# Optimization experiments

Measured on AMD Instinct MI355X. Metric: run time of the kernel, lower is better.

## Reference

```python
import jax, jax.numpy as jnp
import numpy as np
import math

# Static config derived from init_kwargs
B, L, D, H, NL = 256, 256, 128, 2, 2
E = D // H                       # 64
F = L // 2 + 1                   # 129 rfft bins
SR = 0.6                         # sample_ratio (> 1/n_layers)
STEP = (F * (1.0 - SR)) // (NL - 1)          # 51.0, python float floor-div as in torch code
LEFTS = [int(F * (1.0 - SR) - k * STEP) for k in range(NL)]   # [51, 0]
RIGHTS = [int(F - k * STEP) for k in range(NL)]               # [129, 78]
TOPK = max(int(1 * math.log(L)), 1)          # factor=1 -> 5
NUM_TOTAL = 100000                           # user_num + item_num
SPATIAL_RATIO = 0.1
INV_SQRT_E = 1.0 / math.sqrt(E)
INV_SQRT_2 = 1.0 / math.sqrt(2.0)


def setup_inputs() -> dict:
    key = jax.random.key(0)
    ks = jax.random.split(key, 12)
    s = 0.05
    return {
        "paths": jax.random.randint(ks[0], (B, L), 0, NUM_TOTAL),
        "lengths": jax.random.randint(ks[1], (B,), 1, L + 1),
        "degrees": jax.random.randint(ks[2], (B,), 0, 64),
        "training": 1,
        "ego_emb": jax.random.normal(ks[3], (NUM_TOTAL + 1, D), jnp.float32) * s,
        "pos_emb": jax.random.normal(ks[4], (L, D), jnp.float32) * s,
        "Wq": jax.random.normal(ks[5], (NL, D, D), jnp.float32) * s,
        "Wk": jax.random.normal(ks[6], (NL, D, D), jnp.float32) * s,
        "Wv": jax.random.normal(ks[7], (NL, D, D), jnp.float32) * s,
        "Wp": jax.random.normal(ks[8], (NL, D, D), jnp.float32) * s,
        "F1": jax.random.normal(ks[9], (NL, D, 2 * D), jnp.float32) * s,
        "F2": jax.random.normal(ks[10], (NL, 2 * D, D), jnp.float32) * s,
    }


def _hybrid_attention(k, x, mask, Wq, Wk, Wv, Wp):
    # project and split heads: [B,H,E,L]
    def proj(W):
        return (x @ W).reshape(B, L, H, E).transpose(0, 2, 3, 1)
    q, kk, v = proj(Wq), proj(Wk), proj(Wv)
    qf = jnp.fft.rfft(q, axis=-1)   # [B,H,E,F] complex
    kf = jnp.fft.rfft(kk, axis=-1)
    vf = jnp.fft.rfft(v, axis=-1)
    l, r = LEFTS[k], RIGHTS[k]
    # frequency-band attention: band-limited cross-correlation (scatter back == zero-pad)
    res = qf[..., l:r] * jnp.conj(kf[..., l:r])
    box = jnp.zeros(qf.shape, dtype=res.dtype).at[..., l:r].set(res)
    corr = jnp.fft.irfft(box, n=L, axis=-1)          # [B,H,E,L]
    mean_value = jnp.mean(corr, axis=(1, 2))         # [B,L]
    # training branch: global topk delays (shared across batch), roll-based aggregation
    _, delays = jax.lax.top_k(jnp.mean(mean_value, axis=0), TOPK)   # [TOPK]
    weights = mean_value[:, delays]                  # [B,TOPK]
    tmp_corr = jax.nn.softmax(weights, axis=-1)      # [B,TOPK]
    # roll(v, -d) along time == gather at (t + d) % L
    idx = (jnp.arange(L)[None, :] + delays[:, None]) % L            # [TOPK,L]
    gathered = v[:, :, :, idx]                       # [B,H,E,TOPK,L]
    freq = jnp.einsum('bhetl,bt->bhel', gathered, tmp_corr)
    freq = freq.transpose(0, 3, 1, 2).reshape(B, L, D)
    # dual-domain: time attention on band-limited signals (std=True -> same band)
    def band_ifft(f):
        padded = jnp.zeros(f.shape, dtype=f.dtype).at[..., l:r].set(f[..., l:r])
        return jnp.fft.irfft(padded, n=L, axis=-1).transpose(0, 1, 3, 2)   # [B,H,L,E]
    qt, kt, vt = band_ifft(qf), band_ifft(kf), band_ifft(vf)
    scores = jnp.einsum('bhqe,bhke->bhqk', qt, kt) * INV_SQRT_E + mask
    att = jax.nn.softmax(scores, axis=-1)
    spatial = jnp.einsum('bhqk,bhke->bhqe', att, vt).transpose(0, 2, 1, 3).reshape(B, L, D)
    out = (1.0 - SPATIAL_RATIO) * freq + SPATIAL_RATIO * spatial
    return out @ Wp + x


def reference(paths, lengths, degrees, training, ego_emb, pos_emb, Wq, Wk, Wv, Wp, F1, F2):
    del degrees, training  # degrees unused; training branch baked in (training=True)
    x = ego_emb[paths] + pos_emb[None, :, :]         # [B,L,D]
    m = (paths < NUM_TOTAL).astype(jnp.float32)
    mask = ((1.0 - m) * -10000.0)[:, None, None, :]  # [B,1,1,L]
    for k in range(NL):
        a = _hybrid_attention(k, x, mask, Wq[k], Wk[k], Wv[k], Wp[k])
        h = a @ F1[k]
        h = h * 0.5 * (1.0 + jax.lax.erf(h * INV_SQRT_2))   # exact GELU
        x = h @ F2[k]
    # gather last valid position per sequence
    return x[jnp.arange(B), lengths - 1]             # [B,D]
```

## Files before the change

kernel.cpp:

```cpp
#include <hip/hip_runtime.h>
#include <math.h>

#define Bn 256
#define Ln 256
#define Dn 128
#define Hn 2
#define En 64
#define NLn 2
#define TOPKn 5
#define NUM_TOTALn 100000
#define BLD (Bn*Ln*Dn)
#define WT_LAYER 147456

using frag_ab = __attribute__((ext_vector_type(8))) short;
using frag_cd = __attribute__((ext_vector_type(4))) float;

__device__ inline short f2bf(float f) {
    union { float f; unsigned u; } c; c.f = f;
    unsigned r = (c.u + 0x7FFFu + ((c.u >> 16) & 1u)) >> 16;
    return (short)r;
}
__device__ inline float bf2f(short s) {
    union { unsigned u; float f; } c; c.u = ((unsigned)(unsigned short)s) << 16;
    return c.f;
}

__global__ void beacon_kernel(float* out, float v) { out[0] = v; }

__global__ __launch_bounds__(256) void build_G_kernel(short* __restrict__ G) {
    int k = blockIdx.x, t = blockIdx.y, s = threadIdx.x;
    int d = (t - s) & 255;
    int f1 = (k == 0) ? 51 : 1;
    int f2 = (k == 0) ? 127 : 77;
    float acc;
    if (d == 0) {
        acc = 2.0f * (float)(f2 - f1 + 1);
    } else {
        const float c = 3.14159265358979323846f / 256.0f;
        int ahi = (d * (2 * f2 + 1)) & 511;
        int alo = (d * (2 * f1 - 1)) & 511;
        acc = (sinf(c * (float)ahi) - sinf(c * (float)alo)) / sinf(c * (float)d);
    }
    acc += (k == 0) ? ((d & 1) ? -1.0f : 1.0f)
                    : 1.0f;
    G[((size_t)k * 256 + t) * 256 + s] = f2bf(acc * (1.0f / 256.0f));
}

__global__ __launch_bounds__(256) void build_x_kernel(const int* __restrict__ paths,
                                                      const float* __restrict__ ego,
                                                      const float* __restrict__ pos,
                                                      short* __restrict__ x) {
    int base = (blockIdx.x * 256 + threadIdx.x) * 4;
    int d = base & 127;
    int bl = base >> 7;
    int t = bl & 255;
    float4 e = *(const float4*)(ego + (size_t)paths[bl] * Dn + d);
    float4 p = *(const float4*)(pos + t * Dn + d);
    short4 s;
    s.x = f2bf(e.x + p.x); s.y = f2bf(e.y + p.y);
    s.z = f2bf(e.z + p.z); s.w = f2bf(e.w + p.w);
    *(short4*)&x[base] = s;
}

__global__ __launch_bounds__(256) void wtrans_all_kernel(
        const float* __restrict__ Wq, const float* __restrict__ Wk,
        const float* __restrict__ Wv, const float* __restrict__ Wp,
        const float* __restrict__ F1, const float* __restrict__ F2,
        short* __restrict__ Wt) {
    int z = blockIdx.y;
    int idx = blockIdx.x * 256 + threadIdx.x;
    short* WtL = Wt + (size_t)z * WT_LAYER;
    if (idx < 65536) {
        int which = idx >> 14, local = idx & 16383;
        const float* src = (which == 0) ? Wq : (which == 1) ? Wk
                         : (which == 2) ? Wv : Wp;
        float scale = (which == 3) ? 0.1f : 1.0f;
        int n = local & 127, k = local >> 7;
        WtL[(which << 14) + n * 128 + k] = f2bf(scale * src[(size_t)z * 16384 + local]);
    } else if (idx < 98304) {
        int local = idx - 65536;
        int n = local & 255, k = local >> 8;
        WtL[65536 + n * 128 + k] = f2bf(F1[(size_t)z * 32768 + local]);
    } else {
        int local = idx - 98304;
        int n = local & 127, k = local >> 7;
        WtL[98304 + n * 256 + k] = f2bf(F2[(size_t)z * 32768 + local]);
    }
}

template<bool BT_FAST, bool GELU_EPI>
__global__ __launch_bounds__(256)
void mfma_gemm_kernel(const short* A, const short* Bp, short* C, const short* R,
                      int K, int lda, int ldb, int ldc, int ldr,
                      long long sA, long long sB, long long sC, long long sR,
                      long long sCsplit, float alpha, float beta) {
    int bz = blockIdx.z;
    A += (size_t)bz * sA; C += (size_t)bz * sC;
    if (R) R += (size_t)bz * sR;
    const short* Bt = Bp + (size_t)bz * sB;
    const int m0 = blockIdx.x * 128, n0 = blockIdx.y * 128;
    int n0c = n0;
    if (sCsplit) { C += (size_t)blockIdx.y * sCsplit; n0c = 0; }
    __shared__ short As[128 * 40];
    __shared__ short Bs[128 * 40];
    int tid = threadIdx.x;
    int lane = tid & 63, wave = tid >> 6;
    int wr = (wave >> 1) * 64, wc = (wave & 1) * 64;
    int l15 = lane & 15, qd = lane >> 4;

    frag_cd zero4 = {0.f, 0.f, 0.f, 0.f};
    frag_cd acc[4][4];
    #pragma unroll
    for (int i = 0; i < 4; i++)
        #pragma unroll
        for (int j = 0; j < 4; j++) acc[i][j] = zero4;

    int arow = tid >> 1, acg = (tid & 1) * 16;
    int bnrow = tid >> 1, bcg = (tid & 1) * 16;
    int bkk = tid & 31, bnb = (tid >> 5) * 16;

    int4 pa0, pa1, pb0, pb1;
    {
        const short* ap = A + (size_t)(m0 + arow) * lda + acg;
        pa0 = *(const int4*)ap; pa1 = *(const int4*)(ap + 8);
        if (BT_FAST) {
            const short* bp = Bt + (size_t)(n0 + bnrow) * ldb + bcg;
            pb0 = *(const int4*)bp; pb1 = *(const int4*)(bp + 8);
        } else {
            const short* bp = Bt + (size_t)bkk * ldb + n0 + bnb;
            pb0 = *(const int4*)bp; pb1 = *(const int4*)(bp + 8);
        }
    }

    for (int k0 = 0; k0 < K; k0 += 32) {
        __syncthreads();
        *(int4*)&As[arow * 40 + acg] = pa0;
        *(int4*)&As[arow * 40 + acg + 8] = pa1;
        if (BT_FAST) {
            *(int4*)&Bs[bnrow * 40 + bcg] = pb0;
            *(int4*)&Bs[bnrow * 40 + bcg + 8] = pb1;
        } else {
            short tmp[16];
            *(int4*)&tmp[0] = pb0; *(int4*)&tmp[8] = pb1;
            #pragma unroll
            for (int i = 0; i < 16; i++) Bs[(bnb + i) * 40 + bkk] = tmp[i];
        }
        __syncthreads();
        if (k0 + 32 < K) {
            const short* ap = A + (size_t)(m0 + arow) * lda + k0 + 32 + acg;
            pa0 = *(const int4*)ap; pa1 = *(const int4*)(ap + 8);
            if (BT_FAST) {
                const short* bp = Bt + (size_t)(n0 + bnrow) * ldb + k0 + 32 + bcg;
                pb0 = *(const int4*)bp; pb1 = *(const int4*)(bp + 8);
            } else {
                const short* bp = Bt + (size_t)(k0 + 32 + bkk) * ldb + n0 + bnb;
                pb0 = *(const int4*)bp; pb1 = *(const int4*)(bp + 8);
            }
        }
        frag_ab af[4], bf[4];
        #pragma unroll
        for (int ms = 0; ms < 4; ms++)
            af[ms] = *(frag_ab*)&As[(wr + ms * 16 + l15) * 40 + qd * 8];
        #pragma unroll
        for (int ns = 0; ns < 4; ns++)
            bf[ns] = *(frag_ab*)&Bs[(wc + ns * 16 + l15) * 40 + qd * 8];
        #pragma unroll
        for (int ms = 0; ms < 4; ms++)
            #pragma unroll
            for (int ns = 0; ns < 4; ns++)
                acc[ms][ns] = __builtin_amdgcn_mfma_f32_16x16x32_bf16(
                    bf[ns], af[ms], acc[ms][ns], 0, 0, 0);
    }
    #pragma unroll
    for (int ms = 0; ms < 4; ms++) {
        int m = m0 + wr + ms * 16 + l15;
        #pragma unroll
        for (int ns = 0; ns < 4; ns++) {
            int nb = wc + ns * 16 + qd * 4;
            float v[4];
            #pragma unroll
            for (int r = 0; r < 4; r++) v[r] = alpha * acc[ms][ns][r];
            if (R) {
                short4 r4 = *(const short4*)&R[(size_t)m * ldr + n0 + nb];
                v[0] += beta * bf2f(r4.x); v[1] += beta * bf2f(r4.y);
                v[2] += beta * bf2f(r4.z); v[3] += beta * bf2f(r4.w);
            }
            if (GELU_EPI) {
                #pragma unroll
                for (int r = 0; r < 4; r++)
                    v[r] = v[r] * 0.5f * (1.0f + erff(v[r] * 0.70710678118654752f));
            }
            short4 o;
            o.x = f2bf(v[0]); o.y = f2bf(v[1]); o.z = f2bf(v[2]); o.w = f2bf(v[3]);
            *(short4*)&C[(size_t)m * ldc + n0c + nb] = o;
        }
    }
}

static inline void mgemm(hipStream_t s, const short* A, const short* B, short* C,
                         const short* R, int M, int N, int K,
                         int lda, int ldb, int ldc, int ldr,
                         long long sA, long long sB, long long sC, long long sR,
                         int batch, float alpha, float beta, bool btFast, bool gelu,
                         long long sCsplit = 0) {
    dim3 grid(M / 128, N / 128, batch), block(256);
    if (btFast) {
        if (gelu) mfma_gemm_kernel<true, true ><<<grid, block, 0, s>>>(A, B, C, R, K, lda, ldb, ldc, ldr, sA, sB, sC, sR, sCsplit, alpha, beta);
        else      mfma_gemm_kernel<true, false><<<grid, block, 0, s>>>(A, B, C, R, K, lda, ldb, ldc, ldr, sA, sB, sC, sR, sCsplit, alpha, beta);
    } else {
        if (gelu) mfma_gemm_kernel<false, true ><<<grid, block, 0, s>>>(A, B, C, R, K, lda, ldb, ldc, ldr, sA, sB, sC, sR, sCsplit, alpha, beta);
        else      mfma_gemm_kernel<false, false><<<grid, block, 0, s>>>(A, B, C, R, K, lda, ldb, ldc, ldr, sA, sB, sC, sR, sCsplit, alpha, beta);
    }
}

__global__ __launch_bounds__(512)
void filtproj_kernel(const short* __restrict__ G, const short* __restrict__ x,
                     const short* __restrict__ W, short* __restrict__ q) {
    int b = blockIdx.x;
    __shared__ short As[256 * 40];
    __shared__ short Bs[128 * 40];
    __shared__ short xf[256 * 136];
    int tid = threadIdx.x;
    int lane = tid & 63, wave = tid >> 6;
    int wr = (wave & 3) * 64, wc = (wave >> 2) * 64;
    int l15 = lane & 15, qd = lane >> 4;
    const short* xb = x + ((size_t)b << 15);

    frag_cd zero4 = {0.f, 0.f, 0.f, 0.f};
    frag_cd acc[4][4];
    #pragma unroll
    for (int i = 0; i < 4; i++)
        #pragma unroll
        for (int j = 0; j < 4; j++) acc[i][j] = zero4;

    int arow = tid >> 1, acg = (tid & 1) * 16;
    int bkk = tid & 31, bnb = (tid >> 5) * 16;

    int4 pa0, pa1, pb0, pb1;
    {
        const short* ap = G + (size_t)arow * 256 + acg;
        pa0 = *(const int4*)ap; pa1 = *(const int4*)(ap + 8);
        if (tid < 256) {
            const short* bp = xb + (size_t)bkk * 128 + bnb;
            pb0 = *(const int4*)bp; pb1 = *(const int4*)(bp + 8);
        }
    }
    for (int k0 = 0; k0 < 256; k0 += 32) {
        __syncthreads();
        *(int4*)&As[arow * 40 + acg] = pa0;
        *(int4*)&As[arow * 40 + acg + 8] = pa1;
        if (tid < 256) {
            short tmp[16];
            *(int4*)&tmp[0] = pb0; *(int4*)&tmp[8] = pb1;
            #pragma unroll
            for (int i = 0; i < 16; i++) Bs[(bnb + i) * 40 + bkk] = tmp[i];
        }
        __syncthreads();
        if (k0 + 32 < 256) {
            const short* ap = G + (size_t)arow * 256 + k0 + 32 + acg;
            pa0 = *(const int4*)ap; pa1 = *(const int4*)(ap + 8);
            if (tid < 256) {
                const short* bp = xb + (size_t)(k0 + 32 + bkk) * 128 + bnb;
                pb0 = *(const int4*)bp; pb1 = *(const int4*)(bp + 8);
            }
        }
        frag_ab af[4], bf[4];
        #pragma unroll
        for (int ms = 0; ms < 4; ms++)
            af[ms] = *(frag_ab*)&As[(wr + ms * 16 + l15) * 40 + qd * 8];
        #pragma unroll
        for (int ns = 0; ns < 4; ns++)
            bf[ns] = *(frag_ab*)&Bs[(wc + ns * 16 + l15) * 40 + qd * 8];
        #pragma unroll
        for (int ms = 0; ms < 4; ms++)
            #pragma unroll
            for (int ns = 0; ns < 4; ns++)
                acc[ms][ns] = __builtin_amdgcn_mfma_f32_16x16x32_bf16(
                    bf[ns], af[ms], acc[ms][ns], 0, 0, 0);
    }
    #pragma unroll
    for (int ms = 0; ms < 4; ms++) {
        int m = wr + ms * 16 + l15;
        #pragma unroll
        for (int ns = 0; ns < 4; ns++) {
            int nb = wc + ns * 16 + qd * 4;
            short4 o;
            o.x = f2bf(acc[ms][ns][0]); o.y = f2bf(acc[ms][ns][1]);
            o.z = f2bf(acc[ms][ns][2]); o.w = f2bf(acc[ms][ns][3]);
            *(short4*)&xf[m * 136 + nb] = o;
        }
    }

    int brow = tid >> 2, bcg = (tid & 3) * 8;
    #pragma unroll 1
    for (int y = 0; y < 3; y++) {
        const short* Bt = W + y * 16384;
        #pragma unroll
        for (int i = 0; i < 4; i++)
            #pragma unroll
            for (int j = 0; j < 4; j++) acc[i][j] = zero4;
        int4 pb = *(const int4*)(Bt + (size_t)brow * 128 + bcg);
        for (int k0 = 0; k0 < 128; k0 += 32) {
            __syncthreads();
            *(int4*)&Bs[brow * 40 + bcg] = pb;
            __syncthreads();
            if (k0 + 32 < 128)
                pb = *(const int4*)(Bt + (size_t)brow * 128 + k0 + 32 + bcg);
            frag_ab af[4], bf[4];
            #pragma unroll
            for (int ms = 0; ms < 4; ms++)
                af[ms] = *(frag_ab*)&xf[(wr + ms * 16 + l15) * 136 + k0 + qd * 8];
            #pragma unroll
            for (int ns = 0; ns < 4; ns++)
                bf[ns] = *(frag_ab*)&Bs[(wc + ns * 16 + l15) * 40 + qd * 8];
            #pragma unroll
            for (int ms = 0; ms < 4; ms++)
                #pragma unroll
                for (int ns = 0; ns < 4; ns++)
                    acc[ms][ns] = __builtin_amdgcn_mfma_f32_16x16x32_bf16(
                        bf[ns], af[ms], acc[ms][ns], 0, 0, 0);
        }
        short* Cy = q + (size_t)y * BLD + ((size_t)b << 15);
        #pragma unroll
        for (int ms = 0; ms < 4; ms++) {
            int m = wr + ms * 16 + l15;
            #pragma unroll
            for (int ns = 0; ns < 4; ns++) {
                int nb = wc + ns * 16 + qd * 4;
                short4 o;
                o.x = f2bf(acc[ms][ns][0]); o.y = f2bf(acc[ms][ns][1]);
                o.z = f2bf(acc[ms][ns][2]); o.w = f2bf(acc[ms][ns][3]);
                *(short4*)&Cy[(size_t)m * 128 + nb] = o;
            }
        }
    }
}

__global__ __launch_bounds__(512)
void amix_ffn_kernel(const short* __restrict__ x, const short* __restrict__ q,
                     const short* __restrict__ W,
                     const float* __restrict__ tc, const int* __restrict__ delays,
                     short* __restrict__ xout) {
    int b = blockIdx.x;
    __shared__ short aL[256 * 132];
    __shared__ short hA[256 * 132];
    __shared__ short Bs[2][128 * 40];
    int tid = threadIdx.x;
    int lane = tid & 63, wave = tid >> 6;
    int wr = (wave & 3) * 64, wc = (wave >> 2) * 64;
    int l15 = lane & 15, qd = lane >> 4;
    const short* xb = x + ((size_t)b << 15);

    float wj[TOPKn]; int dj[TOPKn];
    #pragma unroll
    for (int j = 0; j < TOPKn; j++) {
        wj[j] = tc[b * TOPKn + j];
        dj[j] = delays[j];
    }

    frag_cd zero4 = {0.f, 0.f, 0.f, 0.f};

    {
        int arow = tid >> 1, acg = (tid & 1) * 16;
        #pragma unroll
        for (int k0 = 0; k0 < 128; k0 += 32) {
            #pragma unroll
            for (int c = 0; c < 2; c++) {
                int col = k0 + acg + c * 8;
                float m8[8] = {0.f, 0.f, 0.f, 0.f, 0.f, 0.f, 0.f, 0.f};
                #pragma unroll
                for (int j = 0; j < TOPKn; j++) {
                    frag_ab v = *(const frag_ab*)(xb + (((arow + dj[j]) & 255) << 7) + col);
                    #pragma unroll
                    for (int i = 0; i < 8; i++) m8[i] += wj[j] * bf2f(v[i]);
                }
                frag_ab o;
                #pragma unroll
                for (int i = 0; i < 8; i++) o[i] = f2bf(m8[i]);
                *(frag_ab*)&hA[arow * 132 + col] = o;
            }
        }
        const short* qb = q + ((size_t)b << 15);
        #pragma unroll
        for (int p = 0; p < 8; p++) {
            int chunk = p * 512 + tid;
            int r = chunk >> 4, cb = (chunk & 15) * 8;
            *(frag_ab*)&aL[r * 132 + cb] = *(const frag_ab*)(qb + (size_t)r * 128 + cb);
        }
    }
    __syncthreads();

    int brow = tid >> 2, bcg = (tid & 3) * 8;

    frag_cd acc[4][4];
    #pragma unroll
    for (int i = 0; i < 4; i++)
        #pragma unroll
        for (int j = 0; j < 4; j++) acc[i][j] = zero4;
    #pragma unroll 1
    for (int pass = 0; pass < 2; pass++) {
        const short* Bt = W + (pass ? 49152 : 131072);
        const short* Asrc = pass ? aL : hA;
        int4 pb = *(const int4*)(Bt + (size_t)brow * 128 + bcg);
        int cur = 0;
        for (int k0 = 0; k0 < 128; k0 += 32, cur ^= 1) {
            *(int4*)&Bs[cur][brow * 40 + bcg] = pb;
            if (k0 + 32 < 128)
                pb = *(const int4*)(Bt + (size_t)brow * 128 + k0 + 32 + bcg);
            __syncthreads();
            frag_ab af[4], bf[4];
            #pragma unroll
            for (int ms = 0; ms < 4; ms++)
                af[ms] = *(frag_ab*)&Asrc[(wr + ms * 16 + l15) * 132 + k0 + qd * 8];
            #pragma unroll
            for (int ns = 0; ns < 4; ns++)
                bf[ns] = *(frag_ab*)&Bs[cur][(wc + ns * 16 + l15) * 40 + qd * 8];
            #pragma unroll
            for (int ms = 0; ms < 4; ms++)
                #pragma unroll
                for (int ns = 0; ns < 4; ns++)
                    acc[ms][ns] = __builtin_amdgcn_mfma_f32_16x16x32_bf16(
                        bf[ns], af[ms], acc[ms][ns], 0, 0, 0);
        }
    }
    __syncthreads();
    #pragma unroll
    for (int ms = 0; ms < 4; ms++) {
        int m = wr + ms * 16 + l15;
        #pragma unroll
        for (int ns = 0; ns < 4; ns++) {
            int nb = wc + ns * 16 + qd * 4;
            short4 r4 = *(const short4*)&xb[(size_t)m * 128 + nb];
            float v[4];
            v[0] = acc[ms][ns][0] + bf2f(r4.x);
            v[1] = acc[ms][ns][1] + bf2f(r4.y);
            v[2] = acc[ms][ns][2] + bf2f(r4.z);
            v[3] = acc[ms][ns][3] + bf2f(r4.w);
            short4 o;
            o.x = f2bf(v[0]); o.y = f2bf(v[1]); o.z = f2bf(v[2]); o.w = f2bf(v[3]);
            *(short4*)&aL[m * 132 + nb] = o;
        }
    }
    __syncthreads();

    const short* F1T = W + 65536;
    const short* F2T = W + 98304;
    frag_cd xacc[4][4];
    #pragma unroll
    for (int i = 0; i < 4; i++)
        #pragma unroll
        for (int j = 0; j < 4; j++) xacc[i][j] = zero4;

    #pragma unroll 1
    for (int half = 0; half < 2; half++) {
        const short* B1 = F1T + (size_t)(half * 128) * 128;
        frag_cd hacc[4][4];
        #pragma unroll
        for (int i = 0; i < 4; i++)
            #pragma unroll
            for (int j = 0; j < 4; j++) hacc[i][j] = zero4;
        {
            int4 pb = *(const int4*)(B1 + (size_t)brow * 128 + bcg);
            int cur = 0;
            for (int k0 = 0; k0 < 128; k0 += 32, cur ^= 1) {
                *(int4*)&Bs[cur][brow * 40 + bcg] = pb;
                if (k0 + 32 < 128)
                    pb = *(const int4*)(B1 + (size_t)brow * 128 + k0 + 32 + bcg);
                __syncthreads();
                frag_ab af[4], bf[4];
                #pragma unroll
                for (int ms = 0; ms < 4; ms++)
                    af[ms] = *(frag_ab*)&aL[(wr + ms * 16 + l15) * 132 + k0 + qd * 8];
                #pragma unroll
                for (int ns = 0; ns < 4; ns++)
                    bf[ns] = *(frag_ab*)&Bs[cur][(wc + ns * 16 + l15) * 40 + qd * 8];
                #pragma unroll
                for (int ms = 0; ms < 4; ms++)
                    #pragma unroll
                    for (int ns = 0; ns < 4; ns++)
                        hacc[ms][ns] = __builtin_amdgcn_mfma_f32_16x16x32_bf16(
                            bf[ns], af[ms], hacc[ms][ns], 0, 0, 0);
            }
        }
        __syncthreads();
        #pragma unroll
        for (int ms = 0; ms < 4; ms++) {
            int m = wr + ms * 16 + l15;
            #pragma unroll
            for (int ns = 0; ns < 4; ns++) {
                int nb = wc + ns * 16 + qd * 4;
                float v[4];
                #pragma unroll
                for (int r = 0; r < 4; r++) {
                    float t = hacc[ms][ns][r];
                    v[r] = t * 0.5f * (1.0f + erff(t * 0.70710678118654752f));
                }
                short4 o;
                o.x = f2bf(v[0]); o.y = f2bf(v[1]);
                o.z = f2bf(v[2]); o.w = f2bf(v[3]);
                *(short4*)&hA[m * 132 + nb] = o;
            }
        }
        __syncthreads();

        {
            int4 pb = *(const int4*)(F2T + (size_t)brow * 256 + half * 128 + bcg);
            int cur = 0;
            for (int k0 = 0; k0 < 128; k0 += 32, cur ^= 1) {
                *(int4*)&Bs[cur][brow * 40 + bcg] = pb;
                if (k0 + 32 < 128)
                    pb = *(const int4*)(F2T + (size_t)brow * 256 + half * 128 + k0 + 32 + bcg);
                __syncthreads();
                frag_ab af[4], bf[4];
                #pragma unroll
                for (int ms = 0; ms < 4; ms++)
                    af[ms] = *(frag_ab*)&hA[(wr + ms * 16 + l15) * 132 + k0 + qd * 8];
                #pragma unroll
                for (int ns = 0; ns < 4; ns++)
                    bf[ns] = *(frag_ab*)&Bs[cur][(wc + ns * 16 + l15) * 40 + qd * 8];
                #pragma unroll
                for (int ms = 0; ms < 4; ms++)
                    #pragma unroll
                    for (int ns = 0; ns < 4; ns++)
                        xacc[ms][ns] = __builtin_amdgcn_mfma_f32_16x16x32_bf16(
                            bf[ns], af[ms], xacc[ms][ns], 0, 0, 0);
            }
        }
    }
    short* xo = xout + ((size_t)b << 15);
    #pragma unroll
    for (int ms = 0; ms < 4; ms++) {
        int m = wr + ms * 16 + l15;
        #pragma unroll
        for (int ns = 0; ns < 4; ns++) {
            int nb = wc + ns * 16 + qd * 4;
            short4 o;
            o.x = f2bf(xacc[ms][ns][0]); o.y = f2bf(xacc[ms][ns][1]);
            o.z = f2bf(xacc[ms][ns][2]); o.w = f2bf(xacc[ms][ns][3]);
            *(short4*)&xo[(size_t)m * 128 + nb] = o;
        }
    }
}

__global__ __launch_bounds__(512, 4) void attn_kernel(short* q,
        const short* __restrict__ kb, const short* __restrict__ vf,
        const int* __restrict__ paths, float* __restrict__ mv2) {
    int h = blockIdx.x, b = blockIdx.y;
    __shared__ short SB[256 * 72];
    __shared__ short ks[64 * 72];
    __shared__ short vT[80 * 72];
    __shared__ float masks[256];
    __shared__ float mvpart[512];
    int tid = threadIdx.x;
    int lane = tid & 63, wave = tid >> 6;
    int l15 = lane & 15, qd = lane >> 4;
    if (tid < 256) masks[tid] = (paths[b * 256 + tid] < NUM_TOTALn) ? 0.0f : -10000.0f;
    {
        int e0 = tid * 2;
        #pragma unroll
        for (int i = 0; i < 2; i++) {
            int e = e0 + i;
            int row = 64 + (e >> 6), col = e & 63;
            vT[row * 72 + col] = (row == 64) ? (short)0x3F80 : (short)0;
        }
    }
    short* qg = q + ((size_t)b << 15) + (size_t)h * 64;
    const short* kg = kb + ((size_t)b << 15) + (size_t)h * 64;
    const short* vg = vf + ((size_t)b << 15) + (size_t)h * 64;

    #pragma unroll
    for (int p = 0; p < 4; p++) {
        int chunk = p * 512 + tid;
        int r = chunk >> 3, cb = (chunk & 7) * 8;
        *(frag_ab*)&SB[r * 72 + cb] = *(const frag_ab*)(qg + (size_t)r * 128 + cb);
    }
    __syncthreads();
    int myrow = wave * 32;
    frag_ab aq[2][2];
    #pragma unroll
    for (int mt = 0; mt < 2; mt++)
        #pragma unroll
        for (int hf = 0; hf < 2; hf++)
            aq[mt][hf] = *(frag_ab*)&SB[(myrow + mt * 16 + l15) * 72 + hf * 32 + qd * 8];

    frag_cd zero4 = {0.f, 0.f, 0.f, 0.f};
    frag_cd oacc[2][5];
    #pragma unroll
    for (int mt = 0; mt < 2; mt++)
        #pragma unroll
        for (int et = 0; et < 5; et++) oacc[mt][et] = zero4;
    float macc = 0.0f;
    int tau = tid & 255, half = tid >> 8;

    for (int jt = 0; jt < 4; jt++) {
        __syncthreads();
        {
            int r = tid >> 3, cb = (tid & 7) * 8;
            *(frag_ab*)&ks[r * 72 + cb] =
                *(const frag_ab*)(kg + (size_t)(jt * 64 + r) * 128 + cb);
            frag_ab v8 = *(const frag_ab*)(vg + (size_t)(jt * 64 + r) * 128 + cb);
            int swz = (((r >> 3) ^ (cb >> 3)) << 3) + (r & 7);
            #pragma unroll
            for (int i = 0; i < 8; i++) vT[(cb + i) * 72 + swz] = v8[i];
        }
        __syncthreads();
        #pragma unroll
        for (int mt = 0; mt < 2; mt++) {
            #pragma unroll
            for (int nt = 0; nt < 4; nt++) {
                frag_ab b0 = *(frag_ab*)&ks[(nt * 16 + l15) * 72 + qd * 8];
                frag_ab b1 = *(frag_ab*)&ks[(nt * 16 + l15) * 72 + 32 + qd * 8];
                frag_cd c = zero4;
                c = __builtin_amdgcn_mfma_f32_16x16x32_bf16(aq[mt][0], b0, c, 0, 0, 0);
                c = __builtin_amdgcn_mfma_f32_16x16x32_bf16(aq[mt][1], b1, c, 0, 0, 0);
                int keyLocal = nt * 16 + l15;
                #pragma unroll
                for (int r = 0; r < 4; r++) {
                    int row = myrow + mt * 16 + qd * 4 + r;
                    int tt = (row - jt * 64 - keyLocal) & 255;
                    SB[tt * 66 + keyLocal] = f2bf(c[r] * 0.125f);
                }
            }
        }
        __syncthreads();
        {
            const int* SD32 = (const int*)&SB[tau * 66 + half * 32];
            #pragma unroll
            for (int i = 0; i < 16; i++) {
                int pk = SD32[i];
                macc += bf2f((short)(pk & 0xFFFF)) + bf2f((short)(pk >> 16));
            }
        }
        #pragma unroll
        for (int mt = 0; mt < 2; mt++) {
            int row = myrow + mt * 16 + l15;
            #pragma unroll
            for (int hf = 0; hf < 2; hf++) {
                int kl0 = hf * 32 + qd * 8;
                frag_ab pfrag;
                #pragma unroll
                for (int j = 0; j < 8; j++) {
                    int kl = kl0 + j;
                    int tt = (row - jt * 64 - kl) & 255;
                    float s = bf2f(SB[tt * 66 + kl]);
                    pfrag[j] = f2bf(__expf(s + masks[jt * 64 + kl]));
                }
                #pragma unroll
                for (int et = 0; et < 5; et++) {
                    int e = et * 16 + l15;
                    int blk = (hf * 4 + qd) ^ ((e >> 3) & 7);
                    frag_ab bv = *(frag_ab*)&vT[e * 72 + (blk << 3)];
                    oacc[mt][et] = __builtin_amdgcn_mfma_f32_16x16x32_bf16(pfrag, bv, oacc[mt][et], 0, 0, 0);
                }
            }
        }
    }
    __syncthreads();
    mvpart[tid] = macc;
    __syncthreads();
    if (tid < 256)
        mv2[(size_t)h * 65536 + b * 256 + tid] =
            (mvpart[tid] + mvpart[tid + 256]) * 0.0625f;
    #pragma unroll
    for (int mt = 0; mt < 2; mt++) {
        #pragma unroll
        for (int r = 0; r < 4; r++) {
            float l = oacc[mt][4][r];
            l = __shfl(l, (lane & 48));
            float inv = 1.0f / l;
            int row = myrow + mt * 16 + qd * 4 + r;
            #pragma unroll
            for (int et = 0; et < 4; et++)
                qg[(size_t)row * 128 + et * 16 + l15] = f2bf(oacc[mt][et][r] * inv);
        }
    }
}

__global__ __launch_bounds__(256) void gm_reduce_kernel(const float* __restrict__ mv2,
                                                        float* __restrict__ gm) {
    int tau = blockIdx.x;
    int b = threadIdx.x;
    __shared__ float red[256];
    red[b] = mv2[b * 256 + tau] + mv2[65536 + b * 256 + tau];
    __syncthreads();
    for (int s = 128; s > 0; s >>= 1) { if (b < s) red[b] += red[b + s]; __syncthreads(); }
    if (b == 0) gm[tau] = red[0] * (1.0f / 256.0f);
}

__global__ __launch_bounds__(256) void topk_softmax_kernel(const float* __restrict__ gm,
                                                           const float* __restrict__ mv2,
                                                           int* __restrict__ delays,
                                                           float* __restrict__ tc) {
    __shared__ float vsh[4];
    __shared__ int ish[4];
    __shared__ int dsh[TOPKn];
    int tid = threadIdx.x;
    int lane = tid & 63, wave = tid >> 6;
    float v = gm[tid];
    for (int t = 0; t < TOPKn; t++) {
        float mv_ = v; int mi = tid;
        #pragma unroll
        for (int s = 32; s > 0; s >>= 1) {
            float v2 = __shfl_xor(mv_, s); int i2 = __shfl_xor(mi, s);
            if (v2 > mv_ || (v2 == mv_ && i2 < mi)) { mv_ = v2; mi = i2; }
        }
        if (lane == 0) { vsh[wave] = mv_; ish[wave] = mi; }
        __syncthreads();
        if (tid == 0) {
            float bv = vsh[0]; int bi = ish[0];
            #pragma unroll
            for (int w = 1; w < 4; w++)
                if (vsh[w] > bv || (vsh[w] == bv && ish[w] < bi)) { bv = vsh[w]; bi = ish[w]; }
            dsh[t] = bi; delays[t] = bi;
        }
        __syncthreads();
        if (tid == dsh[t]) v = -1e30f;
    }
    __syncthreads();
    int b = tid;
    float w[TOPKn];
    float m = -1e30f;
    #pragma unroll
    for (int j = 0; j < TOPKn; j++) {
        w[j] = mv2[b * 256 + dsh[j]] + mv2[65536 + b * 256 + dsh[j]];
        m = fmaxf(m, w[j]);
    }
    float ssum = 0.0f;
    #pragma unroll
    for (int j = 0; j < TOPKn; j++) { w[j] = expf(w[j] - m); ssum += w[j]; }
    #pragma unroll
    for (int j = 0; j < TOPKn; j++) tc[b * TOPKn + j] = w[j] / ssum;
}

__global__ __launch_bounds__(256) void gather_out_kernel(const short* __restrict__ x,
                                                         const int* __restrict__ lengths,
                                                         float* __restrict__ out) {
    int idx = blockIdx.x * 256 + threadIdx.x;
    int d = idx & 127;
    int b = idx >> 7;
    out[idx] = bf2f(x[((size_t)b << 15) + (size_t)(lengths[b] - 1) * Dn + d]);
}

extern "C" void kernel_launch(void* const* d_in, const int* in_sizes, int n_in,
                              void* d_out, int out_size, void* d_ws, size_t ws_size,
                              hipStream_t stream) {
    const int* paths    = (const int*)d_in[0];
    const int* lengths  = (const int*)d_in[1];
    const float* ego    = (const float*)d_in[4];
    const float* pos    = (const float*)d_in[5];
    const float* Wq     = (const float*)d_in[6];
    const float* Wk     = (const float*)d_in[7];
    const float* Wv     = (const float*)d_in[8];
    const float* Wp     = (const float*)d_in[9];
    const float* F1     = (const float*)d_in[10];
    const float* F2     = (const float*)d_in[11];
    float* out = (float*)d_out;

    const size_t need = (size_t)5 * BLD * 2 + 131072 * 2 + 131072 * 4
                        + 256 * 4 + 1280 * 4 + 16 * 4 + (size_t)NLn * WT_LAYER * 2;
    if (ws_size < need) {
        beacon_kernel<<<dim3(1), dim3(1), 0, stream>>>(out, (float)(ws_size >> 20));
        return;
    }

    short* x    = (short*)d_ws;
    short* q    = x + (size_t)1 * BLD;
    short* kb   = x + (size_t)2 * BLD;
    short* vf   = x + (size_t)3 * BLD;
    short* Gb   = x + (size_t)5 * BLD;
    float* mv   = (float*)(Gb + 131072);
    float* gm   = mv + 131072;
    float* tc   = gm + 256;
    int* delays = (int*)(tc + 1280);
    short* Wt   = (short*)(delays + 16);

    build_G_kernel<<<dim3(2, 256), dim3(256), 0, stream>>>(Gb);
    build_x_kernel<<<dim3(BLD / 1024), dim3(256), 0, stream>>>(paths, ego, pos, x);

    wtrans_all_kernel<<<dim3(512, NLn), dim3(256), 0, stream>>>(Wq, Wk, Wv, Wp, F1, F2, Wt);
    mgemm(stream, Wt + 49152, Wt + 32768, Wt + 131072, nullptr,
          128, 128, 128, 128, 128, 128, 0,
          WT_LAYER, WT_LAYER, WT_LAYER, 0, NLn,
          9.0f, 0.0f, false, false);

    for (int k = 0; k < NLn; k++) {
        const short* WtL = Wt + (size_t)k * WT_LAYER;
        filtproj_kernel<<<dim3(256), dim3(512), 0, stream>>>(
            Gb + (size_t)k * 65536, x, WtL, q);

        attn_kernel<<<dim3(2, 256), dim3(512), 0, stream>>>(q, kb, vf, paths, mv);

        gm_reduce_kernel<<<dim3(256), dim3(256), 0, stream>>>(mv, gm);
        topk_softmax_kernel<<<dim3(1), dim3(256), 0, stream>>>(gm, mv, delays, tc);

        amix_ffn_kernel<<<dim3(256), dim3(512), 0, stream>>>(
            x, q, WtL, tc, delays, x);
    }

    gather_out_kernel<<<dim3((Bn * Dn) / 256), dim3(256), 0, stream>>>(x, lengths, out);
}
```

Before: 352.0 us.

## Double amix_ffn block to 1024 threads with smaller per-wave tiles, single-buffer B

Raises the amix_ffn block from 8 to 16 waves. Each wave now computes a 64x32 output tile instead of 64x64, which halves the accumulator registers and gives more latency hiding within each block. The B-tile staging goes from a double buffer to a single buffer, so each k-step now needs two barriers, and only half the threads load B. The extra barriers and a single block per CU (LDS still around 145KB) may offset the gain from more waves.

```diff
diff --git a/kernel.cpp b/kernel.cpp
--- a/kernel.cpp
+++ b/kernel.cpp
@@ -336,7 +336,7 @@
     }
 }
 
-__global__ __launch_bounds__(512)
+__global__ __launch_bounds__(1024)
 void amix_ffn_kernel(const short* __restrict__ x, const short* __restrict__ q,
                      const short* __restrict__ W,
                      const float* __restrict__ tc, const int* __restrict__ delays,
@@ -344,10 +344,10 @@
     int b = blockIdx.x;
     __shared__ short aL[256 * 132];
     __shared__ short hA[256 * 132];
-    __shared__ short Bs[2][128 * 40];
+    __shared__ short Bs[128 * 40];
     int tid = threadIdx.x;
     int lane = tid & 63, wave = tid >> 6;
-    int wr = (wave & 3) * 64, wc = (wave >> 2) * 64;
+    int wr = (wave & 3) * 64, wc = (wave >> 2) * 32;
     int l15 = lane & 15, qd = lane >> 4;
     const short* xb = x + ((size_t)b << 15);
 
@@ -361,29 +361,26 @@
     frag_cd zero4 = {0.f, 0.f, 0.f, 0.f};
 
     {
-        int arow = tid >> 1, acg = (tid & 1) * 16;
+        int arow = tid >> 2, acg = (tid & 3) * 8;
         #pragma unroll
         for (int k0 = 0; k0 < 128; k0 += 32) {
-            #pragma unroll
-            for (int c = 0; c < 2; c++) {
-                int col = k0 + acg + c * 8;
-                float m8[8] = {0.f, 0.f, 0.f, 0.f, 0.f, 0.f, 0.f, 0.f};
-                #pragma unroll
-                for (int j = 0; j < TOPKn; j++) {
-                    frag_ab v = *(const frag_ab*)(xb + (((arow + dj[j]) & 255) << 7) + col);
-                    #pragma unroll
-                    for (int i = 0; i < 8; i++) m8[i] += wj[j] * bf2f(v[i]);
-                }
-                frag_ab o;
-                #pragma unroll
-                for (int i = 0; i < 8; i++) o[i] = f2bf(m8[i]);
-                *(frag_ab*)&hA[arow * 132 + col] = o;
-            }
+            int col = k0 + acg;
+            float m8[8] = {0.f, 0.f, 0.f, 0.f, 0.f, 0.f, 0.f, 0.f};
+            #pragma unroll
+            for (int j = 0; j < TOPKn; j++) {
+                frag_ab v = *(const frag_ab*)(xb + (((arow + dj[j]) & 255) << 7) + col);
+                #pragma unroll
+                for (int i = 0; i < 8; i++) m8[i] += wj[j] * bf2f(v[i]);
+            }
+            frag_ab o;
+            #pragma unroll
+            for (int i = 0; i < 8; i++) o[i] = f2bf(m8[i]);
+            *(frag_ab*)&hA[arow * 132 + col] = o;
         }
         const short* qb = q + ((size_t)b << 15);
         #pragma unroll
-        for (int p = 0; p < 8; p++) {
-            int chunk = p * 512 + tid;
+        for (int p = 0; p < 4; p++) {
+            int chunk = p * 1024 + tid;
             int r = chunk >> 4, cb = (chunk & 15) * 8;
             *(frag_ab*)&aL[r * 132 + cb] = *(const frag_ab*)(qb + (size_t)r * 128 + cb);
         }
@@ -392,33 +389,34 @@
 
     int brow = tid >> 2, bcg = (tid & 3) * 8;
 
-    frag_cd acc[4][4];
+    frag_cd acc[4][2];
     #pragma unroll
     for (int i = 0; i < 4; i++)
         #pragma unroll
-        for (int j = 0; j < 4; j++) acc[i][j] = zero4;
+        for (int j = 0; j < 2; j++) acc[i][j] = zero4;
     #pragma unroll 1
     for (int pass = 0; pass < 2; pass++) {
         const short* Bt = W + (pass ? 49152 : 131072);
         const short* Asrc = pass ? aL : hA;
-        int4 pb = *(const int4*)(Bt + (size_t)brow * 128 + bcg);
-        int cur = 0;
-        for (int k0 = 0; k0 < 128; k0 += 32, cur ^= 1) {
-            *(int4*)&Bs[cur][brow * 40 + bcg] = pb;
-            if (k0 + 32 < 128)
+        int4 pb;
+        if (tid < 512) pb = *(const int4*)(Bt + (size_t)brow * 128 + bcg);
+        for (int k0 = 0; k0 < 128; k0 += 32) {
+            __syncthreads();
+            if (tid < 512) *(int4*)&Bs[brow * 40 + bcg] = pb;
+            __syncthreads();
+            if (tid < 512 && k0 + 32 < 128)
                 pb = *(const int4*)(Bt + (size_t)brow * 128 + k0 + 32 + bcg);
-            __syncthreads();
-            frag_ab af[4], bf[4];
+            frag_ab af[4], bf[2];
             #pragma unroll
             for (int ms = 0; ms < 4; ms++)
                 af[ms] = *(frag_ab*)&Asrc[(wr + ms * 16 + l15) * 132 + k0 + qd * 8];
             #pragma unroll
-            for (int ns = 0; ns < 4; ns++)
-                bf[ns] = *(frag_ab*)&Bs[cur][(wc + ns * 16 + l15) * 40 + qd * 8];
+            for (int ns = 0; ns < 2; ns++)
+                bf[ns] = *(frag_ab*)&Bs[(wc + ns * 16 + l15) * 40 + qd * 8];
             #pragma unroll
             for (int ms = 0; ms < 4; ms++)
                 #pragma unroll
-                for (int ns = 0; ns < 4; ns++)
+                for (int ns = 0; ns < 2; ns++)
                     acc[ms][ns] = __builtin_amdgcn_mfma_f32_16x16x32_bf16(
                         bf[ns], af[ms], acc[ms][ns], 0, 0, 0);
         }
@@ -428,7 +426,7 @@
     for (int ms = 0; ms < 4; ms++) {
         int m = wr + ms * 16 + l15;
         #pragma unroll
-        for (int ns = 0; ns < 4; ns++) {
+        for (int ns = 0; ns < 2; ns++) {
             int nb = wc + ns * 16 + qd * 4;
             short4 r4 = *(const short4*)&xb[(size_t)m * 128 + nb];
             float v[4];
@@ -445,39 +443,40 @@
 
     const short* F1T = W + 65536;
     const short* F2T = W + 98304;
-    frag_cd xacc[4][4];
+    frag_cd xacc[4][2];
     #pragma unroll
     for (int i = 0; i < 4; i++)
         #pragma unroll
-        for (int j = 0; j < 4; j++) xacc[i][j] = zero4;
+        for (int j = 0; j < 2; j++) xacc[i][j] = zero4;
 
     #pragma unroll 1
     for (int half = 0; half < 2; half++) {
         const short* B1 = F1T + (size_t)(half * 128) * 128;
-        frag_cd hacc[4][4];
+        frag_cd hacc[4][2];
         #pragma unroll
         for (int i = 0; i < 4; i++)
             #pragma unroll
-            for (int j = 0; j < 4; j++) hacc[i][j] = zero4;
+            for (int j = 0; j < 2; j++) hacc[i][j] = zero4;
         {
-            int4 pb = *(const int4*)(B1 + (size_t)brow * 128 + bcg);
-            int cur = 0;
-            for (int k0 = 0; k0 < 128; k0 += 32, cur ^= 1) {
-                *(int4*)&Bs[cur][brow * 40 + bcg] = pb;
-                if (k0 + 32 < 128)
+            int4 pb;
+            if (tid < 512) pb = *(const int4*)(B1 + (size_t)brow * 128 + bcg);
+            for (int k0 = 0; k0 < 128; k0 += 32) {
+                __syncthreads();
+                if (tid < 512) *(int4*)&Bs[brow * 40 + bcg] = pb;
+                __syncthreads();
+                if (tid < 512 && k0 + 32 < 128)
                     pb = *(const int4*)(B1 + (size_t)brow * 128 + k0 + 32 + bcg);
-                __syncthreads();
-                frag_ab af[4], bf[4];
+                frag_ab af[4], bf[2];
                 #pragma unroll
                 for (int ms = 0; ms < 4; ms++)
                     af[ms] = *(frag_ab*)&aL[(wr + ms * 16 + l15) * 132 + k0 + qd * 8];
                 #pragma unroll
-                for (int ns = 0; ns < 4; ns++)
-                    bf[ns] = *(frag_ab*)&Bs[cur][(wc + ns * 16 + l15) * 40 + qd * 8];
+                for (int ns = 0; ns < 2; ns++)
+                    bf[ns] = *(frag_ab*)&Bs[(wc + ns * 16 + l15) * 40 + qd * 8];
                 #pragma unroll
                 for (int ms = 0; ms < 4; ms++)
                     #pragma unroll
-                    for (int ns = 0; ns < 4; ns++)
+                    for (int ns = 0; ns < 2; ns++)
                         hacc[ms][ns] = __builtin_amdgcn_mfma_f32_16x16x32_bf16(
                             bf[ns], af[ms], hacc[ms][ns], 0, 0, 0);
             }
@@ -487,7 +486,7 @@
         for (int ms = 0; ms < 4; ms++) {
             int m = wr + ms * 16 + l15;
             #pragma unroll
-            for (int ns = 0; ns < 4; ns++) {
+            for (int ns = 0; ns < 2; ns++) {
                 int nb = wc + ns * 16 + qd * 4;
                 float v[4];
                 #pragma unroll
@@ -504,24 +503,25 @@
         __syncthreads();
 
         {
-            int4 pb = *(const int4*)(F2T + (size_t)brow * 256 + half * 128 + bcg);
-            int cur = 0;
-            for (int k0 = 0; k0 < 128; k0 += 32, cur ^= 1) {
-                *(int4*)&Bs[cur][brow * 40 + bcg] = pb;
-                if (k0 + 32 < 128)
+            int4 pb;
+            if (tid < 512) pb = *(const int4*)(F2T + (size_t)brow * 256 + half * 128 + bcg);
+            for (int k0 = 0; k0 < 128; k0 += 32) {
+                __syncthreads();
+                if (tid < 512) *(int4*)&Bs[brow * 40 + bcg] = pb;
+                __syncthreads();
+                if (tid < 512 && k0 + 32 < 128)
                     pb = *(const int4*)(F2T + (size_t)brow * 256 + half * 128 + k0 + 32 + bcg);
-                __syncthreads();
-                frag_ab af[4], bf[4];
+                frag_ab af[4], bf[2];
                 #pragma unroll
                 for (int ms = 0; ms < 4; ms++)
                     af[ms] = *(frag_ab*)&hA[(wr + ms * 16 + l15) * 132 + k0 + qd * 8];
                 #pragma unroll
-                for (int ns = 0; ns < 4; ns++)
-                    bf[ns] = *(frag_ab*)&Bs[cur][(wc + ns * 16 + l15) * 40 + qd * 8];
+                for (int ns = 0; ns < 2; ns++)
+                    bf[ns] = *(frag_ab*)&Bs[(wc + ns * 16 + l15) * 40 + qd * 8];
                 #pragma unroll
                 for (int ms = 0; ms < 4; ms++)
                     #pragma unroll
-                    for (int ns = 0; ns < 4; ns++)
+                    for (int ns = 0; ns < 2; ns++)
                         xacc[ms][ns] = __builtin_amdgcn_mfma_f32_16x16x32_bf16(
                             bf[ns], af[ms], xacc[ms][ns], 0, 0, 0);
             }
@@ -532,7 +532,7 @@
     for (int ms = 0; ms < 4; ms++) {
         int m = wr + ms * 16 + l15;
         #pragma unroll
-        for (int ns = 0; ns < 4; ns++) {
+        for (int ns = 0; ns < 2; ns++) {
             int nb = wc + ns * 16 + qd * 4;
             short4 o;
             o.x = f2bf(xacc[ms][ns][0]); o.y = f2bf(xacc[ms][ns][1]);
@@ -793,7 +793,7 @@
         gm_reduce_kernel<<<dim3(256), dim3(256), 0, stream>>>(mv, gm);
         topk_softmax_kernel<<<dim3(1), dim3(256), 0, stream>>>(gm, mv, delays, tc);
 
-        amix_ffn_kernel<<<dim3(256), dim3(512), 0, stream>>>(
+        amix_ffn_kernel<<<dim3(256), dim3(1024), 0, stream>>>(
             x, q, WtL, tc, delays, x);
     }
 
```

After: 359.8 us. 1.02x slower.
